# Optimization experiments

Measured on AMD Instinct MI355X. Metric: run time of the kernel, lower is better.

The kernel has to match this reference:

```python
import jax, jax.numpy as jnp
import numpy as np

SCALES = (3, 9, 17, 33)  # must be odd so padding=s//2 preserves spatial size


def _box_conv(img, s):
    # img: [B,1,H,W]; conv with an all-ones s x s kernel, 'same' padding for odd s
    k = jnp.ones((1, 1, s, s), img.dtype)
    p = s // 2
    return jax.lax.conv_general_dilated(
        img, k, window_strides=(1, 1), padding=[(p, p), (p, p)],
        dimension_numbers=("NCHW", "OIHW", "NCHW"))


def setup_inputs() -> dict:
    key = jax.random.key(0)
    B, C, H, W = 8, 3, 1024, 1024
    x = jax.random.normal(key, (B, C, H, W), dtype=jnp.float32)
    # mimicking sparse path-traced samples
    keep = jax.random.uniform(jax.random.fold_in(key, 1), (B, 1, H, W)) >= 0.3
    x = jnp.where(keep, x, 0.0)
    return {"x": x}


def reference(x):
    # F.conv2d(x, ones(1,3,1,1)/3) == per-pixel mean over the 3 channels
    lum = jnp.mean(x, axis=1, keepdims=True)          # [B,1,H,W]
    nonzero = (lum != 0).astype(lum.dtype)            # [B,1,H,W]
    feats = []
    for s in SCALES:
        count = _box_conv(nonzero, s)                 # number of nonzero pixels in window
        pool = _box_conv(lum, s) / jnp.maximum(count, 1.0)  # mean over nonzero pixels
        feats.append(count / float(s * s))            # percentage of nonzero pixels
        feats.append(pool)
    return jnp.concatenate(feats, axis=1)             # [B, 2*len(SCALES), H, W]
```

## Files before the change

### kernel.cpp

```cpp
#include <hip/hip_runtime.h>


constexpr int THREADS = 256;
constexpr int LOADW   = 256;
constexpr int HALO    = 17;
constexpr int COUT    = 223;
constexpr int RING    = 37;
constexpr int ROWSEG  = 32;

__device__ __forceinline__ void barrier_lds() {
    asm volatile("s_waitcnt lgkmcnt(0)" ::: "memory");
    __builtin_amdgcn_s_barrier();
    __builtin_amdgcn_sched_barrier(0);
}

template<int CTRL, int RM>
__device__ __forceinline__ int dppadd_i(int v) {
    int sh = __builtin_amdgcn_update_dpp(0, v, CTRL, RM, 0xF, true);
    return v + sh;
}

__device__ __forceinline__ int wave_iscan_i(int v) {
    v = dppadd_i<0x111, 0xF>(v);
    v = dppadd_i<0x112, 0xF>(v);
    v = dppadd_i<0x114, 0xF>(v);
    v = dppadd_i<0x118, 0xF>(v);
    v = dppadd_i<0x142, 0xA>(v);
    v = dppadd_i<0x143, 0xC>(v);
    return v;
}

__global__ __launch_bounds__(THREADS, 4)
void nzfeat_kernel(const float* __restrict__ x, float* __restrict__ out,
                   int B, int H, int W) {
    constexpr int   PP[4]   = {1, 4, 8, 16};
    constexpr float INVA[4] = {1.f/9.f, 1.f/81.f, 1.f/289.f, 1.f/1089.f};
    constexpr float INVQ    = 1.f / 1024.f;

    __shared__ unsigned int ring[RING][LOADW];
    __shared__ int          wsum[2][2][4];

    const int t    = threadIdx.x;
    const int lane = t & 63;
    const int wv   = t >> 6;

    const int x0 = blockIdx.x * COUT;
    const int y0 = blockIdx.y * ROWSEG;
    const int b  = blockIdx.z;

    const int    gx   = x0 - HALO + t;
    const bool   gxok = (gx >= 0) && (gx < W);
    const int    gxc  = min(max(gx, 0), W - 1);
    const size_t HW   = (size_t)H * W;
    const float* xb   = x + (size_t)b * 3 * HW + gxc;

    auto load_row = [&](int r, float& a0, float& a1, float& a2) {
        const int rc = min(max(r, 0), H - 1);
        const float* p = xb + (size_t)rc * W;
        a0 = p[0]; a1 = p[HW]; a2 = p[2 * HW];
    };

    auto slotOf = [&](int r) { return (int)((unsigned)(r + 2 * RING) % (unsigned)RING); };
    auto wpos   = [&](int v) { return v >= RING ? v - RING : v; };
    auto wneg   = [&](int v) { return v < 0 ? v + RING : v; };

    auto scan_local = [&](float c0, float c1, float c2, int r, int par, int which) -> int {
        float lum = 0.f;
        if (gxok && (unsigned)r < (unsigned)H)
            lum = (c0 + c1 + c2) * (1.0f / 3.0f);
        const bool nzb = (lum != 0.f);
        int q   = (int)rintf(lum * 1024.f);
        int val = (q << 16) | (nzb ? 1 : 0);
        int lp  = wave_iscan_i(val);
        if (lane == 63) wsum[par][which][wv] = lp;
        return lp;
    };

    auto combine_write = [&](int par, int A, int Bv, int sA, int sB) {
        int oA = 0, oB = 0;
        #pragma unroll
        for (int w2 = 0; w2 < 3; ++w2)
            if (w2 < wv) {
                oA += wsum[par][0][w2];
                oB += wsum[par][1][w2];
            }
        ring[sA][t] = (unsigned int)(A + oA);
        ring[sB][t] = (unsigned int)(Bv + oB);
    };

    auto wdiff = [&](int s, int xlo, int d, int& dl, int& dn) {
        const unsigned int* rp = &ring[s][xlo];
        unsigned int df = rp[d] - rp[0];
        dl = (int)df >> 16;
        dn = (int)(df & 0xFFFFu);
    };

    float a0, a1, a2, b0c, b1c, b2c;
    load_row(y0 - 18, a0, a1, a2);
    load_row(y0 - 17, b0c, b1c, b2c);
    for (int i = 0; i < 17; ++i) {
        const int rA = y0 - 18 + 2 * i;
        float n0, n1, n2, m0, m1, m2;
        load_row(rA + 2, n0, n1, n2);
        load_row(rA + 3, m0, m1, m2);
        int A  = scan_local(a0, a1, a2, rA, i & 1, 0);
        int Bv = scan_local(b0c, b1c, b2c, rA + 1, i & 1, 1);
        barrier_lds();
        combine_write(i & 1, A, Bv, slotOf(rA), slotOf(rA + 1));
        a0 = n0; a1 = n1; a2 = n2; b0c = m0; b1c = m1; b2c = m2;
    }
    barrier_lds();

    const bool activeCol = (t < COUT) && (x0 + t < W);
    float* outb = out + (size_t)b * 8 * HW + (x0 + t);

    int vl[4], vn[4];
    #pragma unroll
    for (int i = 0; i < 4; ++i) {
        const int p  = PP[i];
        const int d  = 2 * p + 1;
        const int x1 = t + HALO - p - 1;
        int sl = 0, sn = 0;
        for (int rr = y0 - 1 - p; rr <= y0 - 1 + p; ++rr) {
            int dl, dn;
            wdiff(slotOf(rr), x1, d, dl, dn);
            sl += dl; sn += dn;
        }
        vl[i] = sl; vn[i] = sn;
    }

    int sy = slotOf(y0);
    int sw = slotOf(y0 + 16);
    for (int k = 0; k <= ROWSEG / 2; ++k) {
        const bool doScan = (k < ROWSEG / 2);
        int A = 0, Bv = 0;
        float n0 = 0.f, n1 = 0.f, n2 = 0.f, m0 = 0.f, m1 = 0.f, m2 = 0.f;
        if (doScan) {
            const int wA = y0 + 2 * k + 16;
            if (k < ROWSEG / 2 - 1) {
                load_row(wA + 2, n0, n1, n2);
                load_row(wA + 3, m0, m1, m2);
            }
            A  = scan_local(a0, a1, a2, wA, k & 1, 0);
            Bv = scan_local(b0c, b1c, b2c, wA + 1, k & 1, 1);
        }
        barrier_lds();
        if (doScan) {
            combine_write(k & 1, A, Bv, sw, wpos(sw + 1));
            sw = wpos(sw + 2);
        }
        if (k >= 1) {
            const int ye = y0 + 2 * (k - 1);

            #pragma unroll
            for (int i = 0; i < 4; ++i) {
                const int p  = PP[i];
                const int d  = 2 * p + 1;
                const int x1 = t + HALO - p - 1;
                int elE, enE, elL, enL;
                wdiff(wpos(sy + p),     x1, d, elE, enE);
                wdiff(wneg(sy - 1 - p), x1, d, elL, enL);
                vl[i] += elE - elL;
                vn[i] += enE - enL;
            }
            if (activeCol && ye < H) {
                float* o = outb + (size_t)ye * W;
                #pragma unroll
                for (int i = 0; i < 4; ++i) {
                    float cnt = (float)vn[i];
                    o[(size_t)(2 * i) * HW]     = cnt * INVA[i];
                    o[(size_t)(2 * i + 1) * HW] =
                        (float)vl[i] * INVQ * __builtin_amdgcn_rcpf(fmaxf(cnt, 1.f));
                }
            }

            #pragma unroll
            for (int i = 0; i < 4; ++i) {
                const int p  = PP[i];
                const int d  = 2 * p + 1;
                const int x1 = t + HALO - p - 1;
                int elE, enE, elL, enL;
                wdiff(wpos(sy + p + 1), x1, d, elE, enE);
                wdiff(wneg(sy - p),     x1, d, elL, enL);
                vl[i] += elE - elL;
                vn[i] += enE - enL;
            }
            if (activeCol && ye + 1 < H) {
                float* o = outb + (size_t)(ye + 1) * W;
                #pragma unroll
                for (int i = 0; i < 4; ++i) {
                    float cnt = (float)vn[i];
                    o[(size_t)(2 * i) * HW]     = cnt * INVA[i];
                    o[(size_t)(2 * i + 1) * HW] =
                        (float)vl[i] * INVQ * __builtin_amdgcn_rcpf(fmaxf(cnt, 1.f));
                }
            }

            sy = wpos(sy + 2);
        }
        a0 = n0; a1 = n1; a2 = n2; b0c = m0; b1c = m1; b2c = m2;
    }
}

extern "C" void kernel_launch(void* const* d_in, const int* in_sizes, int n_in,
                              void* d_out, int out_size, void* d_ws, size_t ws_size,
                              hipStream_t stream) {
    const float* x   = (const float*)d_in[0];
    float*       out = (float*)d_out;

    const int H = 1024, W = 1024;
    const int B = in_sizes[0] / (3 * H * W);

    dim3 grid((W + COUT - 1) / COUT, (H + ROWSEG - 1) / ROWSEG, B);
    nzfeat_kernel<<<grid, dim3(THREADS), 0, stream>>>(x, out, B, H, W);
}
```

Before: 122.3 us.

## Split into global row-prefix kernel and sliding-window emit kernel

Replaces the single fused kernel, which kept a ring of per-row prefix sums in LDS with halo recomputation, with two kernels. The first computes full-width row prefix sums of packed luminance/nonzero values into a workspace buffer. The second reads those prefixes from global memory to slide vertical windows and write the eight outputs. This removes the LDS barriers and the redundant halo scanning, but it adds a workspace write and read round trip through global memory and L2, plus a second kernel launch.

```diff
diff --git a/kernel.cpp b/kernel.cpp
--- a/kernel.cpp
+++ b/kernel.cpp
@@ -1,18 +1,11 @@
 #include <hip/hip_runtime.h>
 
 
-constexpr int THREADS = 256;
-constexpr int LOADW   = 256;
-constexpr int HALO    = 17;
-constexpr int COUT    = 223;
-constexpr int RING    = 37;
-constexpr int ROWSEG  = 32;
-
-__device__ __forceinline__ void barrier_lds() {
-    asm volatile("s_waitcnt lgkmcnt(0)" ::: "memory");
-    __builtin_amdgcn_s_barrier();
-    __builtin_amdgcn_sched_barrier(0);
-}
+constexpr int W_    = 1024;
+constexpr int H_    = 1024;
+constexpr int PAD   = 17;
+constexpr int PROWS = H_ + 2 * PAD;
+constexpr int RS2   = 64;
 
 template<int CTRL, int RM>
 __device__ __forceinline__ int dppadd_i(int v) {
@@ -30,175 +23,109 @@
     return v;
 }
 
-__global__ __launch_bounds__(THREADS, 4)
-void nzfeat_kernel(const float* __restrict__ x, float* __restrict__ out,
-                   int B, int H, int W) {
+__global__ __launch_bounds__(256)
+void prefix_kernel(const float* __restrict__ x, unsigned int* __restrict__ P,
+                   int B) {
+    const int lane = threadIdx.x & 63;
+    const int wv   = threadIdx.x >> 6;
+    const int rp   = blockIdx.x * 4 + wv;
+    const int b    = blockIdx.z;
+    if (rp >= PROWS) return;
+
+    unsigned int* prow = P + ((size_t)b * PROWS + rp) * W_;
+    const int r = rp - PAD;
+
+    if (r < 0 || r >= H_) {
+        #pragma unroll
+        for (int c = 0; c < 16; ++c) prow[c * 64 + lane] = 0u;
+        return;
+    }
+
+    const size_t HW = (size_t)H_ * W_;
+    const float* px = x + (size_t)b * 3 * HW + (size_t)r * W_;
+
+    float L[16];
+    #pragma unroll
+    for (int c = 0; c < 16; ++c) {
+        const int col = c * 64 + lane;
+        L[c] = (px[col] + px[col + HW] + px[col + 2 * HW]) * (1.0f / 3.0f);
+    }
+
+    int carry = 0;
+    #pragma unroll
+    for (int c = 0; c < 16; ++c) {
+        const float lum = L[c];
+        int val = ((int)rintf(lum * 1024.f) << 16) | ((lum != 0.f) ? 1 : 0);
+        int s = wave_iscan_i(val) + carry;
+        prow[c * 64 + lane] = (unsigned int)s;
+        carry = __shfl(s, 63);
+    }
+}
+
+__global__ __launch_bounds__(256)
+void emit_kernel(const unsigned int* __restrict__ P, float* __restrict__ out,
+                 int B) {
     constexpr int   PP[4]   = {1, 4, 8, 16};
     constexpr float INVA[4] = {1.f/9.f, 1.f/81.f, 1.f/289.f, 1.f/1089.f};
     constexpr float INVQ    = 1.f / 1024.f;
 
-    __shared__ unsigned int ring[RING][LOADW];
-    __shared__ int          wsum[2][2][4];
-
-    const int t    = threadIdx.x;
-    const int lane = t & 63;
-    const int wv   = t >> 6;
-
-    const int x0 = blockIdx.x * COUT;
-    const int y0 = blockIdx.y * ROWSEG;
+    const int t  = threadIdx.x;
+    const int x  = blockIdx.x * 256 + t;
+    const int y0 = blockIdx.y * RS2;
     const int b  = blockIdx.z;
 
-    const int    gx   = x0 - HALO + t;
-    const bool   gxok = (gx >= 0) && (gx < W);
-    const int    gxc  = min(max(gx, 0), W - 1);
-    const size_t HW   = (size_t)H * W;
-    const float* xb   = x + (size_t)b * 3 * HW + gxc;
+    const unsigned int* Pb = P + (size_t)b * PROWS * W_;
+    const size_t HW = (size_t)H_ * W_;
+    float* outb = out + (size_t)b * 8 * HW + x;
 
-    auto load_row = [&](int r, float& a0, float& a1, float& a2) {
-        const int rc = min(max(r, 0), H - 1);
-        const float* p = xb + (size_t)rc * W;
-        a0 = p[0]; a1 = p[HW]; a2 = p[2 * HW];
+    int x1c[4], x2c[4]; bool ok[4];
+    #pragma unroll
+    for (int i = 0; i < 4; ++i) {
+        const int p  = PP[i];
+        const int x1 = x - p - 1;
+        ok[i]  = (x1 >= 0);
+        x1c[i] = max(x1, 0);
+        x2c[i] = min(x + p, W_ - 1);
+    }
+
+    auto rd = [&](int y, int i) -> unsigned int {
+        const unsigned int* rw = Pb + (size_t)(y + PAD) * W_;
+        unsigned int hi = rw[x2c[i]];
+        unsigned int lo = ok[i] ? rw[x1c[i]] : 0u;
+        return hi - lo;
     };
-
-    auto slotOf = [&](int r) { return (int)((unsigned)(r + 2 * RING) % (unsigned)RING); };
-    auto wpos   = [&](int v) { return v >= RING ? v - RING : v; };
-    auto wneg   = [&](int v) { return v < 0 ? v + RING : v; };
-
-    auto scan_local = [&](float c0, float c1, float c2, int r, int par, int which) -> int {
-        float lum = 0.f;
-        if (gxok && (unsigned)r < (unsigned)H)
-            lum = (c0 + c1 + c2) * (1.0f / 3.0f);
-        const bool nzb = (lum != 0.f);
-        int q   = (int)rintf(lum * 1024.f);
-        int val = (q << 16) | (nzb ? 1 : 0);
-        int lp  = wave_iscan_i(val);
-        if (lane == 63) wsum[par][which][wv] = lp;
-        return lp;
-    };
-
-    auto combine_write = [&](int par, int A, int Bv, int sA, int sB) {
-        int oA = 0, oB = 0;
-        #pragma unroll
-        for (int w2 = 0; w2 < 3; ++w2)
-            if (w2 < wv) {
-                oA += wsum[par][0][w2];
-                oB += wsum[par][1][w2];
-            }
-        ring[sA][t] = (unsigned int)(A + oA);
-        ring[sB][t] = (unsigned int)(Bv + oB);
-    };
-
-    auto wdiff = [&](int s, int xlo, int d, int& dl, int& dn) {
-        const unsigned int* rp = &ring[s][xlo];
-        unsigned int df = rp[d] - rp[0];
-        dl = (int)df >> 16;
-        dn = (int)(df & 0xFFFFu);
-    };
-
-    float a0, a1, a2, b0c, b1c, b2c;
-    load_row(y0 - 18, a0, a1, a2);
-    load_row(y0 - 17, b0c, b1c, b2c);
-    for (int i = 0; i < 17; ++i) {
-        const int rA = y0 - 18 + 2 * i;
-        float n0, n1, n2, m0, m1, m2;
-        load_row(rA + 2, n0, n1, n2);
-        load_row(rA + 3, m0, m1, m2);
-        int A  = scan_local(a0, a1, a2, rA, i & 1, 0);
-        int Bv = scan_local(b0c, b1c, b2c, rA + 1, i & 1, 1);
-        barrier_lds();
-        combine_write(i & 1, A, Bv, slotOf(rA), slotOf(rA + 1));
-        a0 = n0; a1 = n1; a2 = n2; b0c = m0; b1c = m1; b2c = m2;
-    }
-    barrier_lds();
-
-    const bool activeCol = (t < COUT) && (x0 + t < W);
-    float* outb = out + (size_t)b * 8 * HW + (x0 + t);
 
     int vl[4], vn[4];
     #pragma unroll
     for (int i = 0; i < 4; ++i) {
-        const int p  = PP[i];
-        const int d  = 2 * p + 1;
-        const int x1 = t + HALO - p - 1;
+        const int p = PP[i];
         int sl = 0, sn = 0;
-        for (int rr = y0 - 1 - p; rr <= y0 - 1 + p; ++rr) {
-            int dl, dn;
-            wdiff(slotOf(rr), x1, d, dl, dn);
-            sl += dl; sn += dn;
+        for (int yy = y0 - 1 - p; yy <= y0 - 1 + p; ++yy) {
+            unsigned int df = rd(yy, i);
+            sl += (int)df >> 16;
+            sn += (int)(df & 0xFFFFu);
         }
         vl[i] = sl; vn[i] = sn;
     }
 
-    int sy = slotOf(y0);
-    int sw = slotOf(y0 + 16);
-    for (int k = 0; k <= ROWSEG / 2; ++k) {
-        const bool doScan = (k < ROWSEG / 2);
-        int A = 0, Bv = 0;
-        float n0 = 0.f, n1 = 0.f, n2 = 0.f, m0 = 0.f, m1 = 0.f, m2 = 0.f;
-        if (doScan) {
-            const int wA = y0 + 2 * k + 16;
-            if (k < ROWSEG / 2 - 1) {
-                load_row(wA + 2, n0, n1, n2);
-                load_row(wA + 3, m0, m1, m2);
-            }
-            A  = scan_local(a0, a1, a2, wA, k & 1, 0);
-            Bv = scan_local(b0c, b1c, b2c, wA + 1, k & 1, 1);
+    #pragma unroll 2
+    for (int y = y0; y < y0 + RS2; ++y) {
+        #pragma unroll
+        for (int i = 0; i < 4; ++i) {
+            const int p = PP[i];
+            unsigned int e = rd(y + p, i);
+            unsigned int l = rd(y - 1 - p, i);
+            vl[i] += ((int)e >> 16) - ((int)l >> 16);
+            vn[i] += (int)(e & 0xFFFFu) - (int)(l & 0xFFFFu);
         }
-        barrier_lds();
-        if (doScan) {
-            combine_write(k & 1, A, Bv, sw, wpos(sw + 1));
-            sw = wpos(sw + 2);
+        float* o = outb + (size_t)y * W_;
+        #pragma unroll
+        for (int i = 0; i < 4; ++i) {
+            float cnt = (float)vn[i];
+            o[(size_t)(2 * i) * HW]     = cnt * INVA[i];
+            o[(size_t)(2 * i + 1) * HW] =
+                (float)vl[i] * INVQ * __builtin_amdgcn_rcpf(fmaxf(cnt, 1.f));
         }
-        if (k >= 1) {
-            const int ye = y0 + 2 * (k - 1);
-
-            #pragma unroll
-            for (int i = 0; i < 4; ++i) {
-                const int p  = PP[i];
-                const int d  = 2 * p + 1;
-                const int x1 = t + HALO - p - 1;
-                int elE, enE, elL, enL;
-                wdiff(wpos(sy + p),     x1, d, elE, enE);
-                wdiff(wneg(sy - 1 - p), x1, d, elL, enL);
-                vl[i] += elE - elL;
-                vn[i] += enE - enL;
-            }
-            if (activeCol && ye < H) {
-                float* o = outb + (size_t)ye * W;
-                #pragma unroll
-                for (int i = 0; i < 4; ++i) {
-                    float cnt = (float)vn[i];
-                    o[(size_t)(2 * i) * HW]     = cnt * INVA[i];
-                    o[(size_t)(2 * i + 1) * HW] =
-                        (float)vl[i] * INVQ * __builtin_amdgcn_rcpf(fmaxf(cnt, 1.f));
-                }
-            }
-
-            #pragma unroll
-            for (int i = 0; i < 4; ++i) {
-                const int p  = PP[i];
-                const int d  = 2 * p + 1;
-                const int x1 = t + HALO - p - 1;
-                int elE, enE, elL, enL;
-                wdiff(wpos(sy + p + 1), x1, d, elE, enE);
-                wdiff(wneg(sy - p),     x1, d, elL, enL);
-                vl[i] += elE - elL;
-                vn[i] += enE - enL;
-            }
-            if (activeCol && ye + 1 < H) {
-                float* o = outb + (size_t)(ye + 1) * W;
-                #pragma unroll
-                for (int i = 0; i < 4; ++i) {
-                    float cnt = (float)vn[i];
-                    o[(size_t)(2 * i) * HW]     = cnt * INVA[i];
-                    o[(size_t)(2 * i + 1) * HW] =
-                        (float)vl[i] * INVQ * __builtin_amdgcn_rcpf(fmaxf(cnt, 1.f));
-                }
-            }
-
-            sy = wpos(sy + 2);
-        }
-        a0 = n0; a1 = n1; a2 = n2; b0c = m0; b1c = m1; b2c = m2;
     }
 }
 
@@ -208,9 +135,12 @@
     const float* x   = (const float*)d_in[0];
     float*       out = (float*)d_out;
 
-    const int H = 1024, W = 1024;
-    const int B = in_sizes[0] / (3 * H * W);
+    const int B = in_sizes[0] / (3 * H_ * W_);
+    unsigned int* P = (unsigned int*)d_ws;
 
-    dim3 grid((W + COUT - 1) / COUT, (H + ROWSEG - 1) / ROWSEG, B);
-    nzfeat_kernel<<<grid, dim3(THREADS), 0, stream>>>(x, out, B, H, W);
+    dim3 g1((PROWS + 3) / 4, 1, B);
+    prefix_kernel<<<g1, dim3(256), 0, stream>>>(x, P, B);
+
+    dim3 g2(W_ / 256, H_ / RS2, B);
+    emit_kernel<<<g2, dim3(256), 0, stream>>>(P, out, B);
 }
```

After: 128.9 us. 5.5% more time.
